# Performance work log

Measured on AMD Instinct MI355X. Metric: run time of the kernel, lower is better.

Reference implementation:

```python
import jax, jax.numpy as jnp
import numpy as np

B, R, P, DP, DR, N, RK = 4, 256, 64, 384, 512, 48, 24


def _ln(x, w, b, eps=1e-5):
    m = x.mean(-1, keepdims=True)
    v = ((x - m) ** 2).mean(-1, keepdims=True)
    return (x - m) / jnp.sqrt(v + eps) * w + b


def _l2norm(x, eps=1e-6):
    return x / jnp.maximum(jnp.linalg.norm(x, axis=-1, keepdims=True), eps)


def setup_inputs() -> dict:
    key = jax.random.key(0)
    ks = jax.random.split(key, 16)
    s = 0.02
    rnd = lambda k, shp: jax.random.normal(k, shp, jnp.float32) * s
    inp = {
        'patch_tokens': jax.random.normal(ks[0], (B, R, P, DP), jnp.float32),
        'patch_mask': jax.random.randint(ks[1], (B, R, P), 0, 2) > 0,
        'near_mask': jax.random.randint(ks[2], (R, R), 0, 2) > 0,
        'far_mask': jax.random.randint(ks[3], (R, R), 0, 2) > 0,
        'local_pos': rnd(ks[4], (1, 1, P, DP)),
        'gate_ln_w': jnp.ones(DP), 'gate_ln_b': jnp.zeros(DP),
        'gate_w1': rnd(ks[5], (DP, DR)), 'gate_b1': jnp.zeros(DR),
        'gate_w2': rnd(ks[6], (DR, 1)), 'gate_b2': jnp.zeros(1),
        'proj_ln1_w': jnp.ones(DP), 'proj_ln1_b': jnp.zeros(DP),
        'proj_w1': rnd(ks[7], (DP, DR)), 'proj_b1': jnp.zeros(DR),
        'proj_w2': rnd(ks[8], (DR, DR)), 'proj_b2': jnp.zeros(DR),
        'proj_ln2_w': jnp.ones(DR), 'proj_ln2_b': jnp.zeros(DR),
        'in_proj_w': rnd(ks[9], (DR, 2 * DR)),
        'x_proj_w': rnd(ks[10], (DR, RK + 2 * N)),
        'dt_w': rnd(ks[11], (RK, DR)),
        'dt_b': jax.random.uniform(ks[12], (DR,), jnp.float32, -4.0, -2.0),
        'A_log': jnp.tile(jnp.log(jnp.arange(1, N + 1, dtype=jnp.float32))[None, :], (DR, 1)),
        'D_param': jnp.ones(DR),
        'out_proj_w': rnd(ks[13], (DR, DR)),
        'scan_ln_w': jnp.ones(DR), 'scan_ln_b': jnp.zeros(DR),
    }
    return inp


def _forward(patch_tokens, patch_mask, near_mask, far_mask, local_pos,
             gate_ln_w, gate_ln_b, gate_w1, gate_b1, gate_w2, gate_b2,
             proj_ln1_w, proj_ln1_b, proj_w1, proj_b1, proj_w2, proj_b2,
             proj_ln2_w, proj_ln2_b, in_proj_w, x_proj_w, dt_w, dt_b,
             A_log, D_param, out_proj_w, scan_ln_w, scan_ln_b):
    # ---- GatedRegionAggregator ----
    x = patch_tokens + local_pos  # [B,R,P,DP]
    g = _ln(x, gate_ln_w, gate_ln_b)
    g = jax.nn.gelu(g @ gate_w1 + gate_b1, approximate=False)
    logits = (g @ gate_w2 + gate_b2)[..., 0]  # [B,R,P]
    logits = jnp.where(patch_mask, logits, jnp.finfo(logits.dtype).min)
    attn = jax.nn.softmax(logits, axis=-1) * patch_mask
    attn = attn / jnp.maximum(attn.sum(-1, keepdims=True), 1e-6)
    pooled = jnp.einsum('brp,brpd->brd', attn, x)  # [B,R,DP]
    p = _ln(pooled, proj_ln1_w, proj_ln1_b)
    p = jax.nn.gelu(p @ proj_w1 + proj_b1, approximate=False)
    p = _ln(p @ proj_w2 + proj_b2, proj_ln2_w, proj_ln2_b)
    p = jnp.nan_to_num(p, nan=0.0, posinf=1.0, neginf=-1.0)
    region = _l2norm(p)  # [B,R,DR]

    # ---- SlowSelectiveScan1D over region sequence (L = R) ----
    xz = region @ in_proj_w  # [B,L,2*DR]
    u, z = jnp.split(xz, 2, axis=-1)
    prm = u @ x_proj_w  # [B,L,RK+2N]
    dt_raw, Bm, Cm = prm[..., :RK], prm[..., RK:RK + N], prm[..., RK + N:]
    delta = jnp.minimum(jax.nn.softplus(dt_raw @ dt_w + dt_b), 10.0)  # [B,L,DR]
    A = -jnp.minimum(jnp.exp(A_log), 1e4)  # [DR,N]
    dA = jnp.exp(jnp.clip(delta[..., None] * A[None, None], -30.0, 30.0))  # [B,L,DR,N]
    dBu = delta[..., None] * Bm[:, :, None, :] * u[..., None]  # [B,L,DR,N]
    log_cumA = jnp.cumsum(jnp.log(jnp.maximum(dA, 1e-38)), axis=1)
    h = jnp.exp(log_cumA) * jnp.cumsum(dBu * jnp.exp(-log_cumA), axis=1)
    y_seq = jnp.einsum('bln,bldn->bld', Cm, h) + D_param * u
    y = (y_seq * jax.nn.silu(z)) @ out_proj_w
    out = _ln(region + jnp.nan_to_num(y, nan=0.0, posinf=1.0, neginf=-1.0),
              scan_ln_w, scan_ln_b)  # [B,R,DR]

    # ---- topology_loss_static ----
    rt = _l2norm(out.astype(jnp.float32))
    sim = jnp.einsum('brd,bsd->brs', rt, rt)  # [B,R,R]
    near = near_mask.astype(sim.dtype)[None]
    far = far_mask.astype(sim.dtype)[None]
    near_loss = ((1.0 - sim) * near).sum() / jnp.maximum(near.sum(), 1.0)
    far_loss = (jax.nn.relu(sim - 0.2) * far).sum() / jnp.maximum(far.sum(), 1.0)
    return out, near_loss + far_loss


def reference(patch_tokens, patch_mask, near_mask, far_mask, local_pos,
              gate_ln_w, gate_ln_b, gate_w1, gate_b1, gate_w2, gate_b2,
              proj_ln1_w, proj_ln1_b, proj_w1, proj_b1, proj_w2, proj_b2,
              proj_ln2_w, proj_ln2_b, in_proj_w, x_proj_w, dt_w, dt_b,
              A_log, D_param, out_proj_w, scan_ln_w, scan_ln_b):
    return _forward(patch_tokens, patch_mask, near_mask, far_mask, local_pos,
                    gate_ln_w, gate_ln_b, gate_w1, gate_b1, gate_w2, gate_b2,
                    proj_ln1_w, proj_ln1_b, proj_w1, proj_b1, proj_w2, proj_b2,
                    proj_ln2_w, proj_ln2_b, in_proj_w, x_proj_w, dt_w, dt_b,
                    A_log, D_param, out_proj_w, scan_ln_w, scan_ln_b)
```

## Files before the change

kernel.cpp:

```cpp
#include <hip/hip_runtime.h>
#include <hip/hip_bf16.h>
#include <math.h>

#define B_ 4
#define R_ 256
#define P_ 64
#define DP_ 384
#define DR_ 512
#define N_ 48
#define RK_ 24
#define MROWS (B_*R_*P_)
#define REGS  (B_*R_)

typedef unsigned short ushort_t;
typedef __attribute__((ext_vector_type(8))) short bf16x8;
typedef __attribute__((ext_vector_type(4))) float f32x4;

#define GLOAD16(g, l) __builtin_amdgcn_global_load_lds( \
    (const __attribute__((address_space(1))) unsigned int*)(g), \
    (__attribute__((address_space(3))) unsigned int*)(l), 16, 0, 0)

#define OFF_PW1  0
#define OFF_PW2  196608
#define OFF_INPW 458752
#define OFF_XPW  983040
#define OFF_DTW  1044480
#define NW_TOT   1056768

__device__ __forceinline__ float us2f(unsigned short u){
  union { unsigned int i; float f; } x; x.i = ((unsigned int)u) << 16; return x.f;
}
__device__ __forceinline__ unsigned short f2us(float f){
  __hip_bfloat16 h = __float2bfloat16(f);
  return *reinterpret_cast<unsigned short*>(&h);
}
__device__ __forceinline__ float gelu_f(float x){
  float u = x * 0.70710678118654752f;
  float au = fabsf(u);
  float tt = 1.0f / fmaf(0.47047f, au, 1.0f);
  float poly = tt * fmaf(tt, fmaf(tt, 0.7478556f, -0.0958798f), 0.3480242f);
  float erfv = 1.0f - poly * __expf(-au * au);
  erfv = (u < 0.f) ? -erfv : erfv;
  return 0.5f * x * (1.0f + erfv);
}
__device__ __forceinline__ float wred_sum(float v){
#pragma unroll
  for (int m = 1; m < 64; m <<= 1) v += __shfl_xor(v, m, 64);
  return v;
}
__device__ __forceinline__ void block_sum4(float v[4], float* s){
  int lane = threadIdx.x & 63, wid = threadIdx.x >> 6;
#pragma unroll
  for (int i = 0; i < 4; ++i){
    float x = v[i];
#pragma unroll
    for (int m = 1; m < 64; m <<= 1) x += __shfl_xor(x, m, 64);
    if (lane == 0) s[wid * 4 + i] = x;
  }
  __syncthreads();
  if (threadIdx.x < 4){
    float t = 0.f;
    for (int t2 = 0; t2 < 8; ++t2) t += s[t2 * 4 + threadIdx.x];
    s[32 + threadIdx.x] = t;
  }
  __syncthreads();
#pragma unroll
  for (int i = 0; i < 4; ++i) v[i] = s[32 + i];
  __syncthreads();
}

__global__ __launch_bounds__(512) void k_prep(
    const float* __restrict__ gw1, const float* __restrict__ glnw,
    const float* __restrict__ glnb, const float* __restrict__ gb1,
    ushort_t* __restrict__ W1pT, float* __restrict__ s1,
    float* __restrict__ b1p, float* __restrict__ accum){
  __shared__ float pss[8][64], psb[8][64];
  int tid = threadIdx.x, seg = tid >> 6, nl = tid & 63;
  int n = blockIdx.x * 64 + nl;
  if (blockIdx.x == 0 && tid < 4) accum[tid] = 0.f;
  float s = 0.f, sb = 0.f;
  int k0 = seg * 48;
  for (int i = 0; i < 48; ++i){
    int k = k0 + i;
    float w1 = gw1[k * DR_ + n];
    float v = glnw[k] * w1;
    unsigned short vr = f2us(v);
    s  += us2f(vr);
    sb += glnb[k] * w1;
    W1pT[(size_t)n * DP_ + k] = vr;
  }
  pss[seg][nl] = s; psb[seg][nl] = sb;
  __syncthreads();
  if (tid < 64){
    float ts = 0.f, tb = 0.f;
    for (int j = 0; j < 8; ++j){ ts += pss[j][tid]; tb += psb[j][tid]; }
    s1[blockIdx.x * 64 + tid] = ts;
    b1p[blockIdx.x * 64 + tid] = gb1[blockIdx.x * 64 + tid] + tb;
  }
}

__global__ __launch_bounds__(512) void k_cast(
    const float* __restrict__ pw1, const float* __restrict__ pw2,
    const float* __restrict__ inpw, const float* __restrict__ xpw,
    const float* __restrict__ dtw, ushort_t* __restrict__ dst){
  int i = (blockIdx.x * 512 + threadIdx.x) * 4;
  if (i >= NW_TOT) return;
  const float* s; int off;
  if (i < OFF_PW2){ s = pw1; off = OFF_PW1; }
  else if (i < OFF_INPW){ s = pw2; off = OFF_PW2; }
  else if (i < OFF_XPW){ s = inpw; off = OFF_INPW; }
  else if (i < OFF_DTW){ s = xpw; off = OFF_XPW; }
  else { s = dtw; off = OFF_DTW; }
  float4 v = *(const float4*)(s + (i - off));
  ushort_t* d = dst + i;
  d[0] = f2us(v.x); d[1] = f2us(v.y); d[2] = f2us(v.z); d[3] = f2us(v.w);
}

__global__ __launch_bounds__(512) void k_xform(
    const float* __restrict__ pt, const float* __restrict__ lp,
    ushort_t* __restrict__ xb, float* __restrict__ mu, float* __restrict__ rsg){
  int tid = threadIdx.x, w = tid >> 6, lane = tid & 63;
  size_t r = (size_t)blockIdx.x * 8 + w;
  int p = (int)(r & (P_ - 1));
  const float* xr = pt + r * DP_ + lane * 6;
  const float* lr = lp + (size_t)p * DP_ + lane * 6;
  float x[6];
  float s = 0.f, ss = 0.f;
#pragma unroll
  for (int i = 0; i < 6; i += 2){
    float2 a = *(const float2*)(xr + i);
    float2 b = *(const float2*)(lr + i);
    x[i] = a.x + b.x; x[i + 1] = a.y + b.y;
  }
#pragma unroll
  for (int i = 0; i < 6; ++i){ s += x[i]; ss += x[i] * x[i]; }
  s = wred_sum(s); ss = wred_sum(ss);
  if (lane == 0){
    float m = s * (1.f / DP_);
    float var = ss * (1.f / DP_) - m * m;
    mu[r] = m;
    rsg[r] = rsqrtf(var + 1e-5f);
  }
  ushort_t* xw = xb + r * DP_ + lane * 6;
#pragma unroll
  for (int i = 0; i < 6; i += 2){
    ushort2 u2; u2.x = f2us(x[i]); u2.y = f2us(x[i + 1]);
    *(ushort2*)(xw + i) = u2;
  }
}

__global__ __launch_bounds__(1024, 4) void k_gate_pool(
    const ushort_t* __restrict__ xb,
    const ushort_t* __restrict__ BT,
    const float* __restrict__ mu, const float* __restrict__ rsg,
    const float* __restrict__ s1, const float* __restrict__ b1p,
    const float* __restrict__ w2, const int* __restrict__ pmask,
    float* __restrict__ pooled){
  __shared__ __align__(16) ushort_t Abuf[2][128 * 64];
  __shared__ float wpart[16][128];
  __shared__ float logit_lds[128];
  __shared__ float smu[128], srs[128];
  __shared__ float attn2[2][64];
  int tid = threadIdx.x;
  int lane = tid & 63, w = tid >> 6;
  int t = lane & 15, g = lane >> 4;
  long r0 = (long)blockIdx.x * 128;
  if (tid < 128){
    smu[tid] = mu[r0 + tid];
    srs[tid] = rsg[r0 + tid];
  }

  f32x4 acc[8][2];
#pragma unroll
  for (int m = 0; m < 8; ++m)
#pragma unroll
    for (int n = 0; n < 2; ++n) acc[m][n] = (f32x4){0.f, 0.f, 0.f, 0.f};

  int ro = lane >> 3, c = lane & 7;
  int srow = (w << 3) + ro;
  const ushort_t* asrc = xb + (size_t)(r0 + srow) * DP_ + ((c ^ (srow & 7)) << 3);

  GLOAD16(asrc, Abuf[0] + (w << 9));
  __syncthreads();

  for (int kt = 0; kt < 6; ++kt){
    int cb = kt & 1;
    if (kt < 5) GLOAD16(asrc + (kt + 1) * 64, Abuf[cb ^ 1] + (w << 9));
    bf16x8 bfr[2][2];
#pragma unroll
    for (int kk = 0; kk < 2; ++kk)
#pragma unroll
      for (int n = 0; n < 2; ++n){
        int col = w * 32 + n * 16 + t;
        bfr[kk][n] = *(const bf16x8*)(BT + (size_t)col * DP_ + kt * 64 + (kk * 4 + g) * 8);
      }
#pragma unroll
    for (int kk = 0; kk < 2; ++kk){
      int ch = kk * 4 + g;
#pragma unroll
      for (int m = 0; m < 8; ++m){
        int row = m * 16 + t;
        bf16x8 af = *(const bf16x8*)(Abuf[cb] + row * 64 + ((ch ^ (row & 7)) << 3));
#pragma unroll
        for (int n = 0; n < 2; ++n)
          acc[m][n] = __builtin_amdgcn_mfma_f32_16x16x32_bf16(af, bfr[kk][n], acc[m][n], 0, 0, 0);
      }
    }
    __syncthreads();
  }

  float w2c[2], s1c[2], b1c[2];
#pragma unroll
  for (int n = 0; n < 2; ++n){
    int col = w * 32 + n * 16 + t;
    w2c[n] = w2[col]; s1c[n] = s1[col]; b1c[n] = b1p[col];
  }
#pragma unroll
  for (int m = 0; m < 8; ++m){
#pragma unroll
    for (int j = 0; j < 4; ++j){
      int rl = m * 16 + g * 4 + j;
      float mur = smu[rl], rs = srs[rl];
      float part = 0.f;
#pragma unroll
      for (int n = 0; n < 2; ++n){
        float gp = rs * acc[m][n][j] - mur * rs * s1c[n] + b1c[n];
        part += gelu_f(gp) * w2c[n];
      }
#pragma unroll
      for (int msk = 1; msk < 16; msk <<= 1) part += __shfl_xor(part, msk, 64);
      if (t == 0) wpart[w][rl] = part;
    }
  }
  __syncthreads();
  if (tid < 128){
    float s = 0.f;
#pragma unroll
    for (int wi = 0; wi < 16; ++wi) s += wpart[wi][tid];
    logit_lds[tid] = s;
  }
  __syncthreads();

  int half = tid >> 9, lt = tid & 511;
  long rr0 = r0 + half * 64;
  if (lt < 64){
    int mk = pmask[rr0 + lt];
    float lv = logit_lds[half * 64 + lt];
    float lm = mk ? lv : -3.4e38f;
    float M = lm;
#pragma unroll
    for (int m2 = 1; m2 < 64; m2 <<= 1) M = fmaxf(M, __shfl_xor(M, m2, 64));
    float e = mk ? __expf(lv - M) : 0.f;
    float S = e;
#pragma unroll
    for (int m2 = 1; m2 < 64; m2 <<= 1) S += __shfl_xor(S, m2, 64);
    float a = (S > 0.f) ? e / S : 0.f;
    float S2 = a;
#pragma unroll
    for (int m2 = 1; m2 < 64; m2 <<= 1) S2 += __shfl_xor(S2, m2, 64);
    attn2[half][lt] = a / fmaxf(S2, 1e-6f);
  }
  __syncthreads();

  float* pbuf = (float*)Abuf;
  if (lt < 384){
    int pg = lt / 48, cc = lt % 48;
    float a8[8] = {0,0,0,0,0,0,0,0};
#pragma unroll
    for (int i = 0; i < 8; ++i){
      int p = pg + i * 8;
      bf16x8 v = *(const bf16x8*)(xb + (size_t)(rr0 + p) * DP_ + cc * 8);
      float ap = attn2[half][p];
#pragma unroll
      for (int j = 0; j < 8; ++j) a8[j] = fmaf(ap, us2f((unsigned short)v[j]), a8[j]);
    }
#pragma unroll
    for (int j = 0; j < 8; ++j) pbuf[(half * 8 + pg) * DP_ + cc * 8 + j] = a8[j];
  }
  __syncthreads();
  if (lt < 384){
    float s = 0.f;
#pragma unroll
    for (int g2 = 0; g2 < 8; ++g2) s += pbuf[(half * 8 + g2) * DP_ + lt];
    pooled[(long)(2 * blockIdx.x + half) * DP_ + lt] = s;
  }
}

__global__ __launch_bounds__(512, 4) void k_region(
    const float* __restrict__ pooled,
    const float* __restrict__ ln1w, const float* __restrict__ ln1b,
    const ushort_t* __restrict__ wblob, const float* __restrict__ pb1,
    const float* __restrict__ pb2,
    const float* __restrict__ ln2w, const float* __restrict__ ln2b,
    const float* __restrict__ dtb,
    float* __restrict__ region, float* __restrict__ uT, float* __restrict__ zT,
    float* __restrict__ deltaT, float* __restrict__ BmT, float* __restrict__ CmT){
  const ushort_t* pw1b  = wblob + OFF_PW1;
  const ushort_t* pw2b  = wblob + OFF_PW2;
  const ushort_t* inpwb = wblob + OFF_INPW;
  const ushort_t* xpwb  = wblob + OFF_XPW;
  const ushort_t* dtwb  = wblob + OFF_DTW;
  __shared__ float xr[4][DP_];
  __shared__ float p1[4][DR_];
  __shared__ float rg[4][DR_];
  __shared__ float us[4][DR_];
  __shared__ float ps[4][4][128];
  __shared__ float prm[4][RK_ + 2 * N_];
  __shared__ float red[40];
  int tid = threadIdx.x;
  int r0 = blockIdx.x * 4;
  for (int i = tid; i < 4 * DP_; i += 512) xr[i / DP_][i % DP_] = pooled[(long)r0 * DP_ + i];
  __syncthreads();
  float v[4], t4[4];
#pragma unroll
  for (int i = 0; i < 4; ++i){ v[i] = (tid < DP_) ? xr[i][tid] : 0.f; t4[i] = v[i]; }
  block_sum4(t4, red);
  float dv[4];
#pragma unroll
  for (int i = 0; i < 4; ++i){ dv[i] = (tid < DP_) ? (v[i] - t4[i] * (1.f / DP_)) : 0.f; t4[i] = dv[i] * dv[i]; }
  block_sum4(t4, red);
  if (tid < DP_){
    float lw = ln1w[tid], lb = ln1b[tid];
#pragma unroll
    for (int i = 0; i < 4; ++i)
      xr[i][tid] = dv[i] * rsqrtf(t4[i] * (1.f / DP_) + 1e-5f) * lw + lb;
  }
  __syncthreads();
  {
    float pb = pb1[tid];
    float a[4] = {pb, pb, pb, pb};
    for (int k0 = 0; k0 < DP_; k0 += 16){
      ushort_t wv[16];
#pragma unroll
      for (int j = 0; j < 16; ++j) wv[j] = pw1b[(k0 + j) * DR_ + tid];
#pragma unroll
      for (int j = 0; j < 16; ++j){
        float wf = us2f(wv[j]);
#pragma unroll
        for (int i = 0; i < 4; ++i) a[i] = fmaf(xr[i][k0 + j], wf, a[i]);
      }
    }
#pragma unroll
    for (int i = 0; i < 4; ++i) p1[i][tid] = gelu_f(a[i]);
  }
  __syncthreads();
  float qq[4];
  {
    float pb = pb2[tid];
    float a[4] = {pb, pb, pb, pb};
    for (int k0 = 0; k0 < DR_; k0 += 16){
      ushort_t wv[16];
#pragma unroll
      for (int j = 0; j < 16; ++j) wv[j] = pw2b[(k0 + j) * DR_ + tid];
#pragma unroll
      for (int j = 0; j < 16; ++j){
        float wf = us2f(wv[j]);
#pragma unroll
        for (int i = 0; i < 4; ++i) a[i] = fmaf(p1[i][k0 + j], wf, a[i]);
      }
    }
#pragma unroll
    for (int i = 0; i < 4; ++i) qq[i] = a[i];
  }
  {
#pragma unroll
    for (int i = 0; i < 4; ++i) t4[i] = qq[i];
    block_sum4(t4, red);
    float d2[4];
#pragma unroll
    for (int i = 0; i < 4; ++i){ d2[i] = qq[i] - t4[i] * (1.f / DR_); t4[i] = d2[i] * d2[i]; }
    block_sum4(t4, red);
    float lw = ln2w[tid], lb = ln2b[tid];
    float o[4];
#pragma unroll
    for (int i = 0; i < 4; ++i){
      o[i] = d2[i] * rsqrtf(t4[i] * (1.f / DR_) + 1e-5f) * lw + lb;
      if (isnan(o[i])) o[i] = 0.f; else if (isinf(o[i])) o[i] = (o[i] > 0.f) ? 1.f : -1.f;
      t4[i] = o[i] * o[i];
    }
    block_sum4(t4, red);
#pragma unroll
    for (int i = 0; i < 4; ++i){
      float rv = o[i] / fmaxf(sqrtf(t4[i]), 1e-6f);
      rg[i][tid] = rv;
      region[(long)(r0 + i) * DR_ + tid] = rv;
    }
  }
  __syncthreads();
  {
    float ua[4] = {0,0,0,0}, zb[4] = {0,0,0,0};
    for (int k0 = 0; k0 < DR_; k0 += 8){
      ushort_t w1v[8], w2v[8];
#pragma unroll
      for (int j = 0; j < 8; ++j){
        w1v[j] = inpwb[(k0 + j) * 1024 + tid];
        w2v[j] = inpwb[(k0 + j) * 1024 + tid + 512];
      }
#pragma unroll
      for (int j = 0; j < 8; ++j){
        float wa = us2f(w1v[j]), wb = us2f(w2v[j]);
#pragma unroll
        for (int i = 0; i < 4; ++i){
          float x = rg[i][k0 + j];
          ua[i] = fmaf(x, wa, ua[i]); zb[i] = fmaf(x, wb, zb[i]);
        }
      }
    }
#pragma unroll
    for (int i = 0; i < 4; ++i){
      us[i][tid] = ua[i];
      uT[(long)tid * REGS + r0 + i] = ua[i];
      zT[(long)tid * REGS + r0 + i] = zb[i];
    }
  }
  __syncthreads();
  {
    int sseg = tid >> 7, cc = tid & 127;
    float pr[4] = {0,0,0,0};
    if (cc < RK_ + 2 * N_){
      int kb = sseg * 128;
      for (int k0 = kb; k0 < kb + 128; k0 += 16){
        ushort_t wv[16];
#pragma unroll
        for (int j = 0; j < 16; ++j) wv[j] = xpwb[(k0 + j) * (RK_ + 2 * N_) + cc];
#pragma unroll
        for (int j = 0; j < 16; ++j){
          float wf = us2f(wv[j]);
#pragma unroll
          for (int i = 0; i < 4; ++i) pr[i] = fmaf(us[i][k0 + j], wf, pr[i]);
        }
      }
    }
#pragma unroll
    for (int i = 0; i < 4; ++i) ps[sseg][i][cc] = pr[i];
  }
  __syncthreads();
  {
    int rr2 = tid >> 7, cc = tid & 127;
    if (cc < RK_ + 2 * N_)
      prm[rr2][cc] = ps[0][rr2][cc] + ps[1][rr2][cc] + ps[2][rr2][cc] + ps[3][rr2][cc];
  }
  __syncthreads();
#pragma unroll
  for (int r = 0; r < 4; ++r){
    float aa = dtb[tid];
#pragma unroll
    for (int j = 0; j < RK_; ++j) aa = fmaf(prm[r][j], us2f(dtwb[j * DR_ + tid]), aa);
    float sp = (aa > 20.f) ? aa : log1pf(expf(aa));
    deltaT[(long)tid * REGS + r0 + r] = fminf(sp, 10.f);
  }
  if (tid < N_){
#pragma unroll
    for (int r = 0; r < 4; ++r){
      BmT[(long)tid * REGS + r0 + r] = prm[r][RK_ + tid];
      CmT[(long)tid * REGS + r0 + r] = prm[r][RK_ + N_ + tid];
    }
  }
}

__global__ __launch_bounds__(256) void k_scan(
    const float* __restrict__ deltaT, const float* __restrict__ uT,
    const float* __restrict__ zT, const float* __restrict__ BmT,
    const float* __restrict__ CmT, const float* __restrict__ alog,
    const float* __restrict__ Dp, float* __restrict__ ys){
  __shared__ float sAn[N_];
  __shared__ float sA[N_][4];
  __shared__ float sB[N_][4];
  int tid = threadIdx.x, lane = tid & 63, w = tid >> 6;
  int ch = blockIdx.x;
  int b = ch >> 9, d = ch & (DR_ - 1);
  if (tid < N_) sAn[tid] = -fminf(__expf(alog[d * N_ + tid]), 10000.f);
  long col = (long)b * R_ + tid;
  float dl = deltaT[(long)d * REGS + col];
  float uu = uT[(long)d * REGS + col];
  float zz = zT[(long)d * REGS + col];
  float Dd = Dp[d];
  float part = 0.f;
  __syncthreads();
  for (int nc = 0; nc < 6; ++nc){
    float bmv[8], cmv[8];
#pragma unroll
    for (int j = 0; j < 8; ++j){
      bmv[j] = BmT[(long)(nc * 8 + j) * REGS + col];
      cmv[j] = CmT[(long)(nc * 8 + j) * REGS + col];
    }
    float aA[8], aB[8];
#pragma unroll
    for (int j = 0; j < 8; ++j){
      int n = nc * 8 + j;
      float cc = fminf(fmaxf(dl * sAn[n], -30.f), 30.f);
      float a = exp2f(cc * 1.44269504f);
      float bv = dl * bmv[j] * uu;
#pragma unroll
      for (int s = 1; s < 64; s <<= 1){
        float a_sh = __shfl_up(a, (unsigned)s, 64);
        float b_sh = __shfl_up(bv, (unsigned)s, 64);
        float nb = fmaf(a, b_sh, bv);
        float na = a * a_sh;
        if (lane >= s){ bv = nb; a = na; }
      }
      aA[j] = a; aB[j] = bv;
      if (lane == 63){ sA[n][w] = a; sB[n][w] = bv; }
    }
    __syncthreads();
#pragma unroll
    for (int j = 0; j < 8; ++j){
      int n = nc * 8 + j;
      float hin = 0.f;
#pragma unroll
      for (int tt = 0; tt < 3; ++tt){
        if (tt < w) hin = sA[n][tt] * hin + sB[n][tt];
      }
      float h = fmaf(aA[j], hin, aB[j]);
      part = fmaf(cmv[j], h, part);
    }
    if (nc < 5) __syncthreads();
  }
  float yv = part + Dd * uu;
  float sz = zz / (1.f + __expf(-zz));
  ys[col * DR_ + d] = yv * sz;
}

__global__ __launch_bounds__(512) void k_out(
    const float* __restrict__ ys, const float* __restrict__ W,
    const float* __restrict__ region, const float* __restrict__ lnw,
    const float* __restrict__ lnb, float* __restrict__ outp,
    float* __restrict__ rt){
  __shared__ float yr[4][DR_];
  __shared__ float red[40];
  int tid = threadIdx.x;
  int r0 = blockIdx.x * 4;
  for (int i = tid; i < 4 * DR_; i += 512) yr[i >> 9][i & 511] = ys[(long)r0 * DR_ + i];
  __syncthreads();
  float y[4] = {0,0,0,0};
  for (int k0 = 0; k0 < DR_; k0 += 8){
    float wv[8];
#pragma unroll
    for (int j = 0; j < 8; ++j) wv[j] = W[(k0 + j) * DR_ + tid];
#pragma unroll
    for (int j = 0; j < 8; ++j){
#pragma unroll
      for (int i = 0; i < 4; ++i) y[i] = fmaf(yr[i][k0 + j], wv[j], y[i]);
    }
  }
  float v[4], t4[4];
#pragma unroll
  for (int i = 0; i < 4; ++i){
    if (isnan(y[i])) y[i] = 0.f; else if (isinf(y[i])) y[i] = (y[i] > 0.f) ? 1.f : -1.f;
    v[i] = region[(long)(r0 + i) * DR_ + tid] + y[i];
    t4[i] = v[i];
  }
  block_sum4(t4, red);
  float dv[4];
#pragma unroll
  for (int i = 0; i < 4; ++i){ dv[i] = v[i] - t4[i] * (1.f / DR_); t4[i] = dv[i] * dv[i]; }
  block_sum4(t4, red);
  float o[4];
  float lw = lnw[tid], lb = lnb[tid];
#pragma unroll
  for (int i = 0; i < 4; ++i){
    o[i] = dv[i] * rsqrtf(t4[i] * (1.f / DR_) + 1e-5f) * lw + lb;
    outp[(long)(r0 + i) * DR_ + tid] = o[i];
    t4[i] = o[i] * o[i];
  }
  block_sum4(t4, red);
#pragma unroll
  for (int i = 0; i < 4; ++i)
    rt[(long)(r0 + i) * DR_ + tid] = o[i] / fmaxf(sqrtf(t4[i]), 1e-6f);
}

__global__ __launch_bounds__(512) void k_loss(
    const float* __restrict__ rt, const int* __restrict__ nearm,
    const int* __restrict__ farm, float* __restrict__ accum){
  __shared__ __align__(16) float ar[4][DR_];
  __shared__ float ps[2][4][256];
  __shared__ float wsum[8][4];
  int blk = blockIdx.x, tid = threadIdx.x;
  int b = blk >> 6, q0 = (blk & 63) * 4;
  const float* rtb = rt + (long)b * R_ * DR_;
  for (int i = tid; i < 4 * DR_; i += 512) ar[i >> 9][i & 511] = rtb[(long)q0 * DR_ + i];
  __syncthreads();
  int s = tid & 255, h = tid >> 8;
  const float* rsrow = rtb + (long)s * DR_ + h * 256;
  float dq[4] = {0.f, 0.f, 0.f, 0.f};
  for (int k = 0; k < 256; k += 4){
    float4 yv = *(const float4*)(rsrow + k);
#pragma unroll
    for (int q = 0; q < 4; ++q){
      float4 x = *(const float4*)(&ar[q][h * 256 + k]);
      dq[q] += x.x * yv.x + x.y * yv.y + x.z * yv.z + x.w * yv.w;
    }
  }
#pragma unroll
  for (int q = 0; q < 4; ++q) ps[h][q][s] = dq[q];
  __syncthreads();
  float nl = 0.f, fl = 0.f, nc = 0.f, fc = 0.f;
  if (tid < 256){
#pragma unroll
    for (int q = 0; q < 4; ++q){
      float dot = ps[0][q][tid] + ps[1][q][tid];
      int nm = nearm[(q0 + q) * R_ + tid], fm = farm[(q0 + q) * R_ + tid];
      if (nm){ nl += 1.f - dot; if (b == 0) nc += 1.f; }
      if (fm){ fl += fmaxf(dot - 0.2f, 0.f); if (b == 0) fc += 1.f; }
    }
  }
  nl = wred_sum(nl); fl = wred_sum(fl); nc = wred_sum(nc); fc = wred_sum(fc);
  int w = tid >> 6, lane = tid & 63;
  if (lane == 0){ wsum[w][0] = nl; wsum[w][1] = fl; wsum[w][2] = nc; wsum[w][3] = fc; }
  __syncthreads();
  if (tid == 0){
    float a0 = 0, a1 = 0, a2 = 0, a3 = 0;
    for (int i = 0; i < 8; i++){ a0 += wsum[i][0]; a1 += wsum[i][1]; a2 += wsum[i][2]; a3 += wsum[i][3]; }
    atomicAdd(&accum[0], a0); atomicAdd(&accum[1], a1);
    if (b == 0){ atomicAdd(&accum[2], a2); atomicAdd(&accum[3], a3); }
  }
}

__global__ void k_final(const float* __restrict__ accum, float* __restrict__ outp){
  if (threadIdx.x == 0){
    float loss = accum[0] / fmaxf(accum[2], 1.f) + accum[1] / fmaxf(accum[3], 1.f);
    outp[REGS * DR_] = loss;
  }
}

extern "C" void kernel_launch(void* const* d_in, const int* in_sizes, int n_in,
                              void* d_out, int out_size, void* d_ws, size_t ws_size,
                              hipStream_t stream){
  const float* pt    = (const float*)d_in[0];
  const int*   pmask = (const int*)d_in[1];
  const int*   nearm = (const int*)d_in[2];
  const int*   farm  = (const int*)d_in[3];
  const float* lp    = (const float*)d_in[4];
  const float* glnw  = (const float*)d_in[5];
  const float* glnb  = (const float*)d_in[6];
  const float* gw1   = (const float*)d_in[7];
  const float* gb1   = (const float*)d_in[8];
  const float* gw2   = (const float*)d_in[9];
  const float* pln1w = (const float*)d_in[11];
  const float* pln1b = (const float*)d_in[12];
  const float* pw1   = (const float*)d_in[13];
  const float* pb1   = (const float*)d_in[14];
  const float* pw2   = (const float*)d_in[15];
  const float* pb2   = (const float*)d_in[16];
  const float* pln2w = (const float*)d_in[17];
  const float* pln2b = (const float*)d_in[18];
  const float* inpw  = (const float*)d_in[19];
  const float* xpw   = (const float*)d_in[20];
  const float* dtw   = (const float*)d_in[21];
  const float* dtb   = (const float*)d_in[22];
  const float* alog  = (const float*)d_in[23];
  const float* dpar  = (const float*)d_in[24];
  const float* opw   = (const float*)d_in[25];
  const float* slnw  = (const float*)d_in[26];
  const float* slnb  = (const float*)d_in[27];

  char* ws = (char*)d_ws;
  size_t off = 0;
  auto alloc = [&](size_t bytes){ size_t o = off; off += (bytes + 255) & ~(size_t)255; return o; };
  ushort_t* W1pT  = (ushort_t*)(ws + alloc((size_t)DR_ * DP_ * 2));
  float* s1     = (float*)(ws + alloc(DR_ * 4));
  float* b1p    = (float*)(ws + alloc(DR_ * 4));
  ushort_t* wblob = (ushort_t*)(ws + alloc((size_t)NW_TOT * 2));
  ushort_t* xb  = (ushort_t*)(ws + alloc((size_t)MROWS * DP_ * 2));
  float* mu     = (float*)(ws + alloc((size_t)MROWS * 4));
  float* rsg    = (float*)(ws + alloc((size_t)MROWS * 4));
  float* pooled = (float*)(ws + alloc((size_t)REGS * DP_ * 4));
  float* region = (float*)(ws + alloc((size_t)REGS * DR_ * 4));
  float* uT     = (float*)(ws + alloc((size_t)REGS * DR_ * 4));
  float* zT     = (float*)(ws + alloc((size_t)REGS * DR_ * 4));
  float* deltaT = (float*)(ws + alloc((size_t)REGS * DR_ * 4));
  float* BmT    = (float*)(ws + alloc((size_t)REGS * N_ * 4));
  float* CmT    = (float*)(ws + alloc((size_t)REGS * N_ * 4));
  float* ys     = (float*)(ws + alloc((size_t)REGS * DR_ * 4));
  float* rt     = (float*)(ws + alloc((size_t)REGS * DR_ * 4));
  float* accum  = (float*)(ws + alloc(4 * 4));

  float* outp = (float*)d_out;

  k_prep<<<dim3(8), dim3(512), 0, stream>>>(gw1, glnw, glnb, gb1, W1pT, s1, b1p, accum);
  k_cast<<<dim3((NW_TOT / 4 + 511) / 512), dim3(512), 0, stream>>>(pw1, pw2, inpw, xpw, dtw, wblob);
  k_xform<<<dim3(MROWS / 8), dim3(512), 0, stream>>>(pt, lp, xb, mu, rsg);
  k_gate_pool<<<dim3(MROWS / 128), dim3(1024), 0, stream>>>(xb, W1pT, mu, rsg, s1, b1p, gw2, pmask, pooled);
  k_region<<<dim3(REGS / 4), dim3(512), 0, stream>>>(pooled, pln1w, pln1b, wblob, pb1, pb2, pln2w, pln2b,
                                                     dtb, region, uT, zT, deltaT, BmT, CmT);
  k_scan<<<dim3(B_ * DR_), dim3(256), 0, stream>>>(deltaT, uT, zT, BmT, CmT, alog, dpar, ys);
  k_out<<<dim3(REGS / 4), dim3(512), 0, stream>>>(ys, opw, region, slnw, slnb, outp, rt);
  k_loss<<<dim3(REGS / 4), dim3(512), 0, stream>>>(rt, nearm, farm, accum);
  k_final<<<dim3(1), dim3(64), 0, stream>>>(accum, outp);
}
```

Baseline: 311.8 us.

## Double k_region block to 1024 threads with split-K partial sums

k_region now launches 1024 threads per block instead of 512. Each GEMV-like stage splits the K dimension across the two thread halves and combines partial sums in shared memory. The in_proj stage gives each thread one of the 1024 output columns, and x_proj uses 8 K-segments instead of 4. The aim is more parallelism and latency hiding in a kernel with only 256 blocks, at the cost of extra shared-memory reductions, barriers and a wider block reduction.

After: 319.8 us. 1.03x slower.

```diff
diff --git a/kernel.cpp b/kernel.cpp
--- a/kernel.cpp
+++ b/kernel.cpp
@@ -66,6 +66,26 @@
   __syncthreads();
 #pragma unroll
   for (int i = 0; i < 4; ++i) v[i] = s[32 + i];
+  __syncthreads();
+}
+__device__ __forceinline__ void bsum4w16(float v[4], float* s){
+  int lane = threadIdx.x & 63, wid = threadIdx.x >> 6;
+#pragma unroll
+  for (int i = 0; i < 4; ++i){
+    float x = v[i];
+#pragma unroll
+    for (int m = 1; m < 64; m <<= 1) x += __shfl_xor(x, m, 64);
+    if (lane == 0) s[wid * 4 + i] = x;
+  }
+  __syncthreads();
+  if (threadIdx.x < 4){
+    float t = 0.f;
+    for (int j = 0; j < 16; ++j) t += s[j * 4 + threadIdx.x];
+    s[64 + threadIdx.x] = t;
+  }
+  __syncthreads();
+#pragma unroll
+  for (int i = 0; i < 4; ++i) v[i] = s[64 + i];
   __syncthreads();
 }
 
@@ -286,7 +306,7 @@
   }
 }
 
-__global__ __launch_bounds__(512, 4) void k_region(
+__global__ __launch_bounds__(1024, 4) void k_region(
     const float* __restrict__ pooled,
     const float* __restrict__ ln1w, const float* __restrict__ ln1b,
     const ushort_t* __restrict__ wblob, const float* __restrict__ pb1,
@@ -304,21 +324,22 @@
   __shared__ float p1[4][DR_];
   __shared__ float rg[4][DR_];
   __shared__ float us[4][DR_];
-  __shared__ float ps[4][4][128];
-  __shared__ float prm[4][RK_ + 2 * N_];
-  __shared__ float red[40];
+  __shared__ float ps[4096];
+  __shared__ float prm[4][128];
+  __shared__ float red[72];
   int tid = threadIdx.x;
+  int col = tid & 511, half = tid >> 9;
   int r0 = blockIdx.x * 4;
-  for (int i = tid; i < 4 * DP_; i += 512) xr[i / DP_][i % DP_] = pooled[(long)r0 * DP_ + i];
+  for (int i = tid; i < 4 * DP_; i += 1024) xr[i / DP_][i % DP_] = pooled[(long)r0 * DP_ + i];
   __syncthreads();
   float v[4], t4[4];
 #pragma unroll
   for (int i = 0; i < 4; ++i){ v[i] = (tid < DP_) ? xr[i][tid] : 0.f; t4[i] = v[i]; }
-  block_sum4(t4, red);
+  bsum4w16(t4, red);
   float dv[4];
 #pragma unroll
   for (int i = 0; i < 4; ++i){ dv[i] = (tid < DP_) ? (v[i] - t4[i] * (1.f / DP_)) : 0.f; t4[i] = dv[i] * dv[i]; }
-  block_sum4(t4, red);
+  bsum4w16(t4, red);
   if (tid < DP_){
     float lw = ln1w[tid], lb = ln1b[tid];
 #pragma unroll
@@ -327,12 +348,12 @@
   }
   __syncthreads();
   {
-    float pb = pb1[tid];
-    float a[4] = {pb, pb, pb, pb};
-    for (int k0 = 0; k0 < DP_; k0 += 16){
+    float a[4] = {0.f, 0.f, 0.f, 0.f};
+    int kb = half * 192;
+    for (int k0 = kb; k0 < kb + 192; k0 += 16){
       ushort_t wv[16];
 #pragma unroll
-      for (int j = 0; j < 16; ++j) wv[j] = pw1b[(k0 + j) * DR_ + tid];
+      for (int j = 0; j < 16; ++j) wv[j] = pw1b[(k0 + j) * DR_ + col];
 #pragma unroll
       for (int j = 0; j < 16; ++j){
         float wf = us2f(wv[j]);
@@ -341,17 +362,23 @@
       }
     }
 #pragma unroll
-    for (int i = 0; i < 4; ++i) p1[i][tid] = gelu_f(a[i]);
-  }
-  __syncthreads();
-  float qq[4];
+    for (int i = 0; i < 4; ++i) ps[half * 2048 + i * 512 + col] = a[i];
+  }
+  __syncthreads();
+  if (tid < DR_){
+    float pb = pb1[tid];
+#pragma unroll
+    for (int i = 0; i < 4; ++i)
+      p1[i][tid] = gelu_f(ps[i * 512 + tid] + ps[2048 + i * 512 + tid] + pb);
+  }
+  __syncthreads();
   {
-    float pb = pb2[tid];
-    float a[4] = {pb, pb, pb, pb};
-    for (int k0 = 0; k0 < DR_; k0 += 16){
+    float a[4] = {0.f, 0.f, 0.f, 0.f};
+    int kb = half * 256;
+    for (int k0 = kb; k0 < kb + 256; k0 += 16){
       ushort_t wv[16];
 #pragma unroll
-      for (int j = 0; j < 16; ++j) wv[j] = pw2b[(k0 + j) * DR_ + tid];
+      for (int j = 0; j < 16; ++j) wv[j] = pw2b[(k0 + j) * DR_ + col];
 #pragma unroll
       for (int j = 0; j < 16; ++j){
         float wf = us2f(wv[j]);
@@ -360,66 +387,75 @@
       }
     }
 #pragma unroll
-    for (int i = 0; i < 4; ++i) qq[i] = a[i];
-  }
+    for (int i = 0; i < 4; ++i) ps[half * 2048 + i * 512 + col] = a[i];
+  }
+  __syncthreads();
+  float qq[4];
+#pragma unroll
+  for (int i = 0; i < 4; ++i)
+    qq[i] = (tid < DR_) ? (ps[i * 512 + tid] + ps[2048 + i * 512 + tid] + pb2[tid]) : 0.f;
   {
 #pragma unroll
     for (int i = 0; i < 4; ++i) t4[i] = qq[i];
-    block_sum4(t4, red);
+    bsum4w16(t4, red);
     float d2[4];
 #pragma unroll
-    for (int i = 0; i < 4; ++i){ d2[i] = qq[i] - t4[i] * (1.f / DR_); t4[i] = d2[i] * d2[i]; }
-    block_sum4(t4, red);
-    float lw = ln2w[tid], lb = ln2b[tid];
+    for (int i = 0; i < 4; ++i){
+      d2[i] = (tid < DR_) ? (qq[i] - t4[i] * (1.f / DR_)) : 0.f;
+      t4[i] = d2[i] * d2[i];
+    }
+    bsum4w16(t4, red);
     float o[4];
+    float lw = (tid < DR_) ? ln2w[tid] : 0.f, lb = (tid < DR_) ? ln2b[tid] : 0.f;
 #pragma unroll
     for (int i = 0; i < 4; ++i){
       o[i] = d2[i] * rsqrtf(t4[i] * (1.f / DR_) + 1e-5f) * lw + lb;
       if (isnan(o[i])) o[i] = 0.f; else if (isinf(o[i])) o[i] = (o[i] > 0.f) ? 1.f : -1.f;
-      t4[i] = o[i] * o[i];
-    }
-    block_sum4(t4, red);
-#pragma unroll
-    for (int i = 0; i < 4; ++i){
-      float rv = o[i] / fmaxf(sqrtf(t4[i]), 1e-6f);
-      rg[i][tid] = rv;
-      region[(long)(r0 + i) * DR_ + tid] = rv;
+      t4[i] = (tid < DR_) ? o[i] * o[i] : 0.f;
+    }
+    bsum4w16(t4, red);
+    if (tid < DR_){
+#pragma unroll
+      for (int i = 0; i < 4; ++i){
+        float rv = o[i] / fmaxf(sqrtf(t4[i]), 1e-6f);
+        rg[i][tid] = rv;
+        region[(long)(r0 + i) * DR_ + tid] = rv;
+      }
     }
   }
   __syncthreads();
   {
-    float ua[4] = {0,0,0,0}, zb[4] = {0,0,0,0};
-    for (int k0 = 0; k0 < DR_; k0 += 8){
-      ushort_t w1v[8], w2v[8];
-#pragma unroll
-      for (int j = 0; j < 8; ++j){
-        w1v[j] = inpwb[(k0 + j) * 1024 + tid];
-        w2v[j] = inpwb[(k0 + j) * 1024 + tid + 512];
-      }
-#pragma unroll
-      for (int j = 0; j < 8; ++j){
-        float wa = us2f(w1v[j]), wb = us2f(w2v[j]);
-#pragma unroll
-        for (int i = 0; i < 4; ++i){
-          float x = rg[i][k0 + j];
-          ua[i] = fmaf(x, wa, ua[i]); zb[i] = fmaf(x, wb, zb[i]);
-        }
-      }
-    }
-#pragma unroll
-    for (int i = 0; i < 4; ++i){
-      us[i][tid] = ua[i];
-      uT[(long)tid * REGS + r0 + i] = ua[i];
-      zT[(long)tid * REGS + r0 + i] = zb[i];
+    float a[4] = {0.f, 0.f, 0.f, 0.f};
+    for (int k0 = 0; k0 < DR_; k0 += 16){
+      ushort_t wv[16];
+#pragma unroll
+      for (int j = 0; j < 16; ++j) wv[j] = inpwb[(k0 + j) * 1024 + tid];
+#pragma unroll
+      for (int j = 0; j < 16; ++j){
+        float wf = us2f(wv[j]);
+#pragma unroll
+        for (int i = 0; i < 4; ++i) a[i] = fmaf(rg[i][k0 + j], wf, a[i]);
+      }
+    }
+    if (tid < DR_){
+#pragma unroll
+      for (int i = 0; i < 4; ++i){
+        us[i][tid] = a[i];
+        uT[(long)tid * REGS + r0 + i] = a[i];
+      }
+    } else {
+#pragma unroll
+      for (int i = 0; i < 4; ++i)
+        zT[(long)(tid - DR_) * REGS + r0 + i] = a[i];
     }
   }
   __syncthreads();
   {
-    int sseg = tid >> 7, cc = tid & 127;
-    float pr[4] = {0,0,0,0};
+    int seg = tid >> 7, cc = tid & 127;
+    float pr[4] = {0.f, 0.f, 0.f, 0.f};
     if (cc < RK_ + 2 * N_){
-      int kb = sseg * 128;
-      for (int k0 = kb; k0 < kb + 128; k0 += 16){
+      int kb = seg * 64;
+      for (int k0 = kb; k0 < kb + 64; k0 += 16){
         ushort_t wv[16];
 #pragma unroll
         for (int j = 0; j < 16; ++j) wv[j] = xpwb[(k0 + j) * (RK_ + 2 * N_) + cc];
@@ -432,22 +468,28 @@
       }
     }
 #pragma unroll
-    for (int i = 0; i < 4; ++i) ps[sseg][i][cc] = pr[i];
-  }
-  __syncthreads();
-  {
-    int rr2 = tid >> 7, cc = tid & 127;
-    if (cc < RK_ + 2 * N_)
-      prm[rr2][cc] = ps[0][rr2][cc] + ps[1][rr2][cc] + ps[2][rr2][cc] + ps[3][rr2][cc];
-  }
-  __syncthreads();
-#pragma unroll
-  for (int r = 0; r < 4; ++r){
-    float aa = dtb[tid];
-#pragma unroll
-    for (int j = 0; j < RK_; ++j) aa = fmaf(prm[r][j], us2f(dtwb[j * DR_ + tid]), aa);
-    float sp = (aa > 20.f) ? aa : log1pf(expf(aa));
-    deltaT[(long)tid * REGS + r0 + r] = fminf(sp, 10.f);
+    for (int i = 0; i < 4; ++i) ps[seg * 512 + i * 128 + cc] = pr[i];
+  }
+  __syncthreads();
+  if (tid < 512){
+    int rr = tid >> 7, cc = tid & 127;
+    if (cc < RK_ + 2 * N_){
+      float s = 0.f;
+#pragma unroll
+      for (int seg = 0; seg < 8; ++seg) s += ps[seg * 512 + rr * 128 + cc];
+      prm[rr][cc] = s;
+    }
+  }
+  __syncthreads();
+  if (tid < DR_){
+#pragma unroll
+    for (int r = 0; r < 4; ++r){
+      float aa = dtb[tid];
+#pragma unroll
+      for (int j = 0; j < RK_; ++j) aa = fmaf(prm[r][j], us2f(dtwb[j * DR_ + tid]), aa);
+      float sp = (aa > 20.f) ? aa : log1pf(expf(aa));
+      deltaT[(long)tid * REGS + r0 + r] = fminf(sp, 10.f);
+    }
   }
   if (tid < N_){
 #pragma unroll
@@ -681,8 +723,8 @@
   k_cast<<<dim3((NW_TOT / 4 + 511) / 512), dim3(512), 0, stream>>>(pw1, pw2, inpw, xpw, dtw, wblob);
   k_xform<<<dim3(MROWS / 8), dim3(512), 0, stream>>>(pt, lp, xb, mu, rsg);
   k_gate_pool<<<dim3(MROWS / 128), dim3(1024), 0, stream>>>(xb, W1pT, mu, rsg, s1, b1p, gw2, pmask, pooled);
-  k_region<<<dim3(REGS / 4), dim3(512), 0, stream>>>(pooled, pln1w, pln1b, wblob, pb1, pb2, pln2w, pln2b,
-                                                     dtb, region, uT, zT, deltaT, BmT, CmT);
+  k_region<<<dim3(REGS / 4), dim3(1024), 0, stream>>>(pooled, pln1w, pln1b, wblob, pb1, pb2, pln2w, pln2b,
+                                                      dtb, region, uT, zT, deltaT, BmT, CmT);
   k_scan<<<dim3(B_ * DR_), dim3(256), 0, stream>>>(deltaT, uT, zT, BmT, CmT, alog, dpar, ys);
   k_out<<<dim3(REGS / 4), dim3(512), 0, stream>>>(ys, opw, region, slnw, slnb, outp, rt);
   k_loss<<<dim3(REGS / 4), dim3(512), 0, stream>>>(rt, nearm, farm, accum);
```
